# Kernel tuning notes

Measured on AMD Instinct MI355X. Metric: run time of the kernel, lower is better.

The kernel has to match this reference:

```python
import jax, jax.numpy as jnp
import numpy as np

B, L, E, H, D, DFF = 2, 2048, 1024, 16, 64, 4096
SCALE = D ** 0.5


def rmsnorm(x):
    # NOTE: original uses mean(x*x)**0.5 with no eps and no learned scale
    rms = jnp.sqrt(jnp.mean(x * x, axis=-1, keepdims=True))
    return x / rms


def alibi_matrix():
    i = jnp.arange(L)
    dists = -jnp.abs(i[None, :] - i[:, None]).astype(jnp.float32)  # [L, L]
    slopes = 2.0 ** (-jnp.linspace(1.0, 8.0, H))                   # [H]
    alibi = slopes[:, None, None] * dists                          # [H, L, L]
    causal = jnp.tril(jnp.ones((L, L), dtype=bool))
    return jnp.where(causal[None], alibi, -jnp.inf)[None]          # [1, H, L, L]


def setup_inputs() -> dict:
    key = jax.random.key(0)
    ks = jax.random.split(key, 16)
    s = 0.02
    return {
        "X": jax.random.normal(ks[0], (B, L, E), jnp.float32),
        "encoder_out": jax.random.normal(ks[1], (B, L, E), jnp.float32),
        # self-attention params
        "Wqkv": jax.random.normal(ks[2], (E, 3 * H * D), jnp.float32) * s,
        "bqkv": jnp.zeros((3 * H * D,), jnp.float32),
        "Wo_sa": jax.random.normal(ks[3], (H * D, E), jnp.float32) * s,
        "bo_sa": jnp.zeros((E,), jnp.float32),
        # cross-attention params (computed by torch module but its forward returns X, so unused)
        "Wq": jax.random.normal(ks[4], (E, H * D), jnp.float32) * s,
        "bq": jnp.zeros((H * D,), jnp.float32),
        "Wkv": jax.random.normal(ks[5], (E, 2 * H * D), jnp.float32) * s,
        "bkv": jnp.zeros((2 * H * D,), jnp.float32),
        "Wo_ca": jax.random.normal(ks[6], (H * D, E), jnp.float32) * s,
        "bo_ca": jnp.zeros((E,), jnp.float32),
        # GLU FFN params (bias=False)
        "Ww": jax.random.normal(ks[7], (E, DFF), jnp.float32) * s,
        "Wv": jax.random.normal(ks[8], (E, DFF), jnp.float32) * s,
        "Wout": jax.random.normal(ks[9], (DFF, E), jnp.float32) * s,
    }


def reference(X, encoder_out, Wqkv, bqkv, Wo_sa, bo_sa, Wq, bq, Wkv, bkv,
              Wo_ca, bo_ca, Ww, Wv, Wout):
    alibi = alibi_matrix()

    # ---- self-attention (pre-norm + residual) ----
    h = rmsnorm(X)
    qkv = (h @ Wqkv + bqkv).reshape(B, L, H, 3, D)
    Q, K, V = qkv[..., 0, :], qkv[..., 1, :], qkv[..., 2, :]      # [B, L, H, D]
    scores = jnp.einsum('blhd,bmhd->bhlm', Q, K) / SCALE + alibi  # [B, H, L, L]
    attn = jax.nn.softmax(scores, axis=-1)
    ctx = jnp.einsum('bhlm,bmhd->blhd', attn, V).reshape(B, L, H * D)
    X = X + ctx @ Wo_sa + bo_sa

    # ---- cross-attention stage ----
    # Faithful to source: CrossAttention.forward returns its input X (the
    # normalized tensor) rather than the attention output, so this block is
    # X + rmsnorm(X). Cross-attn params never affect the output.
    X = X + rmsnorm(X)

    # ---- GLU FFN (pre-norm + residual), exact (erf) GELU as in torch F.gelu ----
    h = rmsnorm(X)
    ff = jax.nn.gelu(h @ Ww, approximate=False) * (h @ Wv)
    X = X + ff @ Wout
    return X
```

## Files before the change

kernel.cpp:

```cpp
#include <hip/hip_runtime.h>

#define B_SZ 2
#define L_SEQ 2048
#define E_DIM 1024
#define NH 16
#define DH 64
#define DFF_DIM 4096
#define ROWS (B_SZ * L_SEQ)
#define NCID 80

typedef __attribute__((ext_vector_type(8))) short short8;
typedef __attribute__((ext_vector_type(4))) float f32x4;

__device__ __forceinline__ short f2bf(float f) {
  unsigned u = __builtin_bit_cast(unsigned, f);
  u = (u + 0x7FFFu + ((u >> 16) & 1u)) >> 16;
  return (short)u;
}
__device__ __forceinline__ float bf2f(short s) {
  unsigned u = ((unsigned)(unsigned short)s) << 16;
  return __builtin_bit_cast(float, u);
}

__device__ __forceinline__ void async_copy16(const void* g, void* l) {
  __builtin_amdgcn_global_load_lds(
      (const __attribute__((address_space(1))) void*)g,
      (__attribute__((address_space(3))) void*)l, 16, 0, 0);
}

__device__ __forceinline__ float block_sum256(float v) {
  __shared__ float sbuf[4];
#pragma unroll
  for (int off = 32; off > 0; off >>= 1) v += __shfl_xor(v, off, 64);
  int lane = threadIdx.x & 63, w = threadIdx.x >> 6;
  if (lane == 0) sbuf[w] = v;
  __syncthreads();
  return sbuf[0] + sbuf[1] + sbuf[2] + sbuf[3];
}

__global__ __launch_bounds__(256) void prep_all(
    const float* __restrict__ Wqkv, const float* __restrict__ Wo,
    const float* __restrict__ Ww, const float* __restrict__ Wv,
    const float* __restrict__ Wout, const float* __restrict__ X,
    short* __restrict__ WqkvT, short* __restrict__ WoT,
    short* __restrict__ Bcat, short* __restrict__ WoutT,
    short* __restrict__ H) {
  __shared__ float tile[32][33];
  int b = blockIdx.x;
  if (b < 16384) {
    const float* W;
    short* Wt;
    int K, N, poff, bx, by;
    if (b < 3072) {
      W = Wqkv; Wt = WqkvT; K = 1024; N = 3072; poff = -1;
      bx = b % 96; by = b / 96;
    } else if (b < 4096) {
      int c = b - 3072;
      W = Wo; Wt = WoT; K = 1024; N = 1024; poff = -1;
      bx = c & 31; by = c >> 5;
    } else if (b < 8192) {
      int c = b - 4096;
      W = Ww; Wt = Bcat; K = 1024; N = 4096; poff = 0;
      bx = c & 127; by = c >> 7;
    } else if (b < 12288) {
      int c = b - 8192;
      W = Wv; Wt = Bcat; K = 1024; N = 4096; poff = 64;
      bx = c & 127; by = c >> 7;
    } else {
      int c = b - 12288;
      W = Wout; Wt = WoutT; K = 4096; N = 1024; poff = -1;
      bx = c & 31; by = c >> 5;
    }
    int n0 = bx * 32, k0 = by * 32;
    int tx = threadIdx.x & 31, ty = threadIdx.x >> 5;
#pragma unroll
    for (int i = 0; i < 4; i++)
      tile[ty + 8 * i][tx] = W[(size_t)(k0 + ty + 8 * i) * N + n0 + tx];
    __syncthreads();
#pragma unroll
    for (int i = 0; i < 4; i++) {
      int n = n0 + ty + 8 * i;
      int orow = (poff < 0) ? n : ((n >> 6) * 128 + (n & 63) + poff);
      Wt[(size_t)orow * K + k0 + tx] = f2bf(tile[tx][ty + 8 * i]);
    }
  } else {
    size_t row = b - 16384;
    float4 v = ((const float4*)(X + row * E_DIM))[threadIdx.x];
    float ss = v.x * v.x + v.y * v.y + v.z * v.z + v.w * v.w;
    ss = block_sum256(ss);
    float inv = rsqrtf(ss * (1.0f / E_DIM));
    short* h = H + row * E_DIM + (size_t)threadIdx.x * 4;
    h[0] = f2bf(v.x * inv);
    h[1] = f2bf(v.y * inv);
    h[2] = f2bf(v.z * inv);
    h[3] = f2bf(v.w * inv);
  }
}

__global__ __launch_bounds__(256) void resid_rms_fused(
    const float* __restrict__ X, const float* __restrict__ P0,
    const float* __restrict__ P1, const float* __restrict__ bias,
    float* __restrict__ Xout, short* __restrict__ H) {
  size_t row = blockIdx.x;
  int t = threadIdx.x;
  float4 v = ((const float4*)(X + row * E_DIM))[t];
  float4 a = ((const float4*)(P0 + row * E_DIM))[t];
  float4 b = ((const float4*)(P1 + row * E_DIM))[t];
  float4 c = ((const float4*)bias)[t];
  v.x += a.x + b.x + c.x;
  v.y += a.y + b.y + c.y;
  v.z += a.z + b.z + c.z;
  v.w += a.w + b.w + c.w;
  float ss = v.x * v.x + v.y * v.y + v.z * v.z + v.w * v.w;
  ss = block_sum256(ss);
  float inv = rsqrtf(ss * (1.0f / E_DIM));
  float4 o;
  o.x = v.x * (1.0f + inv);
  o.y = v.y * (1.0f + inv);
  o.z = v.z * (1.0f + inv);
  o.w = v.w * (1.0f + inv);
  ((float4*)(Xout + row * E_DIM))[t] = o;
  short* h = H + row * E_DIM + (size_t)t * 4;
  h[0] = f2bf(v.x * inv);
  h[1] = f2bf(v.y * inv);
  h[2] = f2bf(v.z * inv);
  h[3] = f2bf(v.w * inv);
}

__global__ __launch_bounds__(256) void add2_k(const float* __restrict__ X2,
                                              const float* __restrict__ P0,
                                              const float* __restrict__ P1,
                                              float* __restrict__ out) {
  size_t i = (size_t)blockIdx.x * 256 + threadIdx.x;
  float4 v = ((const float4*)X2)[i];
  float4 a = ((const float4*)P0)[i];
  float4 b = ((const float4*)P1)[i];
  v.x += a.x + b.x;
  v.y += a.y + b.y;
  v.z += a.z + b.z;
  v.w += a.w + b.w;
  ((float4*)out)[i] = v;
}

__global__ __launch_bounds__(256, 2) void gemm_bt(
    const short* __restrict__ A, const short* __restrict__ Bt,
    const float* __restrict__ bias, const float* __restrict__ res,
    void* __restrict__ out, int M, int N, int K, int epi, int ksplit) {
  __shared__ short smem[128 * 32 * 4];
  short* As0 = smem;
  short* Bs0 = smem + 4096;
  short* As1 = smem + 8192;
  short* Bs1 = smem + 12288;
  int t = threadIdx.x;
  int lane = t & 63;
  int quad = lane >> 4, l16 = lane & 15;
  int wave = t >> 6;
  int wr = wave >> 1, wc = wave & 1;
  int m0 = blockIdx.y * 128, n0 = blockIdx.x * 128;
  int klen = K / ksplit;
  int kstart = blockIdx.z * klen;

  f32x4 acc[4][4];
#pragma unroll
  for (int i = 0; i < 4; i++)
#pragma unroll
    for (int j = 0; j < 4; j++) acc[i][j] = (f32x4){0.f, 0.f, 0.f, 0.f};

  for (int k0 = kstart; k0 < kstart + klen; k0 += 64) {
    __syncthreads();
#pragma unroll
    for (int p = 0; p < 2; p++) {
      int s = p * 256 + t;
      int mm = s >> 2, kk = (s & 3) * 8;
      const short* ag = A + (size_t)(m0 + mm) * K + k0 + kk;
      const short* bg = Bt + (size_t)(n0 + mm) * K + k0 + kk;
      async_copy16(ag, As0 + (size_t)s * 8);
      async_copy16(bg, Bs0 + (size_t)s * 8);
      async_copy16(ag + 32, As1 + (size_t)s * 8);
      async_copy16(bg + 32, Bs1 + (size_t)s * 8);
    }
    __syncthreads();
#pragma unroll
    for (int half = 0; half < 2; half++) {
      const short* As = half ? As1 : As0;
      const short* Bs = half ? Bs1 : Bs0;
      short8 af[4], bfv[4];
#pragma unroll
      for (int i = 0; i < 4; i++) {
        af[i] = *(const short8*)&As[(wr * 64 + i * 16 + l16) * 32 + quad * 8];
        bfv[i] = *(const short8*)&Bs[(wc * 64 + i * 16 + l16) * 32 + quad * 8];
      }
#pragma unroll
      for (int mi = 0; mi < 4; mi++)
#pragma unroll
        for (int ni = 0; ni < 4; ni++)
          acc[mi][ni] = __builtin_amdgcn_mfma_f32_16x16x32_bf16(
              af[mi], bfv[ni], acc[mi][ni], 0, 0, 0);
    }
  }

  if (epi == 5) {
    __syncthreads();
    short* xbuf = smem;
    if (wc == 0) {
#pragma unroll
      for (int mi = 0; mi < 4; mi++)
#pragma unroll
        for (int ni = 0; ni < 4; ni++)
#pragma unroll
          for (int r = 0; r < 4; r++) {
            int rowl = wr * 64 + mi * 16 + quad * 4 + r;
            float v = acc[mi][ni][r];
            float g = 0.5f * v * (1.0f + erff(v * 0.70710678118654752f));
            xbuf[rowl * 68 + ni * 16 + l16] = f2bf(g);
          }
    }
    __syncthreads();
    if (wc == 1) {
      short* FF = (short*)out;
#pragma unroll
      for (int mi = 0; mi < 4; mi++)
#pragma unroll
        for (int ni = 0; ni < 4; ni++)
#pragma unroll
          for (int r = 0; r < 4; r++) {
            int rowl = wr * 64 + mi * 16 + quad * 4 + r;
            int coll = ni * 16 + l16;
            float w = bf2f(xbuf[rowl * 68 + coll]);
            FF[(size_t)(m0 + rowl) * DFF_DIM + blockIdx.x * 64 + coll] =
                f2bf(w * acc[mi][ni][r]);
          }
    }
    return;
  }

#pragma unroll
  for (int mi = 0; mi < 4; mi++) {
#pragma unroll
    for (int ni = 0; ni < 4; ni++) {
      int col = n0 + wc * 64 + ni * 16 + l16;
      float bv = bias ? bias[col] : 0.0f;
#pragma unroll
      for (int r = 0; r < 4; r++) {
        int row = m0 + wr * 64 + mi * 16 + quad * 4 + r;
        size_t idx = (size_t)row * N + col;
        float v = acc[mi][ni][r] + bv;
        if (epi == 0) {
          ((short*)out)[idx] = f2bf(v);
        } else if (epi == 3) {
          ((float*)out)[idx] = v + res[idx];
        } else {
          float* po = (float*)out + (size_t)blockIdx.z * ((size_t)M * N);
          po[idx] = v;
        }
      }
    }
  }
}

__global__ __launch_bounds__(256) void kv_prep(const short* __restrict__ qkv,
                                               short* __restrict__ Kh,
                                               short* __restrict__ VTh) {
  int lt = blockIdx.x, bh = blockIdx.y;
  int b = bh >> 4, h = bh & 15;
  __shared__ short vtile[64 * 72];
  int t = threadIdx.x;
  int r = t >> 3, c = (t & 7) * 8;
  const short* base =
      qkv + (size_t)(b * L_SEQ + lt * 64) * (3 * NH * DH) + h * (3 * DH);
#pragma unroll
  for (int p = 0; p < 2; p++) {
    int row = r + p * 32;
    short8 kv = *(const short8*)(base + (size_t)row * (3 * NH * DH) + DH + c);
    *(short8*)(Kh + ((size_t)bh * L_SEQ + lt * 64 + row) * DH + c) = kv;
    short8 vv =
        *(const short8*)(base + (size_t)row * (3 * NH * DH) + 2 * DH + c);
    *(short8*)&vtile[row * 72 + c] = vv;
  }
  __syncthreads();
#pragma unroll
  for (int p = 0; p < 2; p++) {
    int d = r + p * 32;
    short8 o;
#pragma unroll
    for (int u = 0; u < 8; u++) o[u] = vtile[(c + u) * 72 + d];
    *(short8*)(VTh + ((size_t)bh * DH + d) * L_SEQ + lt * 64 + c) = o;
  }
}

__global__ __launch_bounds__(256) void attn_k(const short* __restrict__ qkv,
                                              const short* __restrict__ Kh,
                                              const short* __restrict__ VTh,
                                              float* __restrict__ OP,
                                              float* __restrict__ RS) {
  int cid = blockIdx.x;
  int bh = blockIdx.y;
  int b = bh >> 4, h = bh & 15;
  int qt, ch;
  if (cid < 8) {
    qt = cid; ch = 0;
  } else if (cid < 24) {
    qt = 8 + ((cid - 8) >> 1); ch = (cid - 8) & 1;
  } else if (cid < 48) {
    qt = 16 + (cid - 24) / 3; ch = (cid - 24) % 3;
  } else {
    qt = 24 + ((cid - 48) >> 2); ch = (cid - 48) & 3;
  }
  int t0 = ch * 8;
  int tend = min(t0 + 8, qt + 1);

  int t = threadIdx.x;
  int wave = t >> 6, lane = t & 63;
  int quad = lane >> 4, l16 = lane & 15;

  __shared__ short kt[64 * 72];
  __shared__ short vt[64 * 72];
  __shared__ short pb[4 * 16 * 70];

  const float slope = exp2f(-(1.0f + (7.0f / 15.0f) * (float)h));
  const size_t rowstride = 3 * NH * DH;
  const short* qbase = qkv + (size_t)(b * L_SEQ) * rowstride + h * (3 * DH);
  int iw = qt * 64 + wave * 16;

  short8 qf[2];
  {
    const short* qp = qbase + (size_t)(iw + l16) * rowstride + quad * 8;
    qf[0] = *(const short8*)(qp);
    qf[1] = *(const short8*)(qp + 32);
  }

  f32x4 o[4];
#pragma unroll
  for (int i = 0; i < 4; i++) o[i] = (f32x4){0.f, 0.f, 0.f, 0.f};
  float rs[4] = {0.f, 0.f, 0.f, 0.f};
  float crow[4];
  int irow[4];
#pragma unroll
  for (int r = 0; r < 4; r++) {
    irow[r] = iw + quad * 4 + r;
    crow[r] = -slope * (float)irow[r] - 8.0f;
  }

  int sr = t >> 3, sc = (t & 7) * 8;
  const short* kg = Kh + (size_t)bh * L_SEQ * DH;
  const short* vg = VTh + (size_t)bh * DH * L_SEQ;
  short8 kreg[2], vreg[2];
  auto loadKV = [&](int j0) {
    kreg[0] = *(const short8*)(kg + (size_t)(j0 + sr) * DH + sc);
    kreg[1] = *(const short8*)(kg + (size_t)(j0 + sr + 32) * DH + sc);
    vreg[0] = *(const short8*)(vg + (size_t)sr * L_SEQ + j0 + sc);
    vreg[1] = *(const short8*)(vg + (size_t)(sr + 32) * L_SEQ + j0 + sc);
  };
  loadKV(t0 * 64);

  short* pw = &pb[wave * 16 * 70];
  for (int tix = t0; tix < tend; ++tix) {
    int j0 = tix * 64;
    __syncthreads();
    *(short8*)&kt[sr * 72 + sc] = kreg[0];
    *(short8*)&kt[(sr + 32) * 72 + sc] = kreg[1];
    *(short8*)&vt[sr * 72 + sc] = vreg[0];
    *(short8*)&vt[(sr + 32) * 72 + sc] = vreg[1];
    __syncthreads();
    if (tix + 1 < tend) loadKV(j0 + 64);

    f32x4 s[4];
#pragma unroll
    for (int nt = 0; nt < 4; nt++) {
      f32x4 a = (f32x4){0.f, 0.f, 0.f, 0.f};
#pragma unroll
      for (int ks = 0; ks < 2; ks++) {
        short8 bf =
            *(const short8*)&kt[(nt * 16 + l16) * 72 + ks * 32 + quad * 8];
        a = __builtin_amdgcn_mfma_f32_16x16x32_bf16(qf[ks], bf, a, 0, 0, 0);
      }
      s[nt] = a;
    }
    bool diag = (tix == qt);
#pragma unroll
    for (int nt = 0; nt < 4; nt++) {
      int j = j0 + nt * 16 + l16;
      float jb = slope * (float)j;
#pragma unroll
      for (int r = 0; r < 4; r++) {
        float v = __builtin_fmaf(s[nt][r], 0.125f, jb + crow[r]);
        if (diag && j > irow[r]) v = -1e30f;
        float p = __expf(v);
        rs[r] += p;
        pw[(quad * 4 + r) * 70 + nt * 16 + l16] = f2bf(p);
      }
    }
    short8 pf[2];
    pf[0] = *(const short8*)&pw[l16 * 70 + quad * 8];
    pf[1] = *(const short8*)&pw[l16 * 70 + 32 + quad * 8];
#pragma unroll
    for (int nt = 0; nt < 4; nt++) {
#pragma unroll
      for (int ks = 0; ks < 2; ks++) {
        short8 bv =
            *(const short8*)&vt[(nt * 16 + l16) * 72 + ks * 32 + quad * 8];
        o[nt] = __builtin_amdgcn_mfma_f32_16x16x32_bf16(pf[ks], bv, o[nt], 0,
                                                        0, 0);
      }
    }
  }
  float* op = OP + ((size_t)bh * NCID + cid) * 64 * 64;
  float* rsp = RS + ((size_t)bh * NCID + cid) * 64;
#pragma unroll
  for (int r = 0; r < 4; r++) {
#pragma unroll
    for (int off = 1; off < 16; off <<= 1) rs[r] += __shfl_xor(rs[r], off, 64);
    int rowl = wave * 16 + quad * 4 + r;
#pragma unroll
    for (int nt = 0; nt < 4; nt++) op[rowl * 64 + nt * 16 + l16] = o[nt][r];
    if (l16 == 0) rsp[rowl] = rs[r];
  }
}

__global__ __launch_bounds__(256) void attn_merge(const float* __restrict__ OP,
                                                  const float* __restrict__ RS,
                                                  short* __restrict__ ctx) {
  int row = blockIdx.x;
  int b = row >> 11, i = row & 2047;
  int qt = i >> 6, rowin = i & 63;
  int base, nch;
  if (qt < 8) {
    base = qt; nch = 1;
  } else if (qt < 16) {
    base = 8 + 2 * (qt - 8); nch = 2;
  } else if (qt < 24) {
    base = 24 + 3 * (qt - 16); nch = 3;
  } else {
    base = 48 + 4 * (qt - 24); nch = 4;
  }
  int t = threadIdx.x;
  int col = t * 4;
  int h = col >> 6;
  int bh = b * NH + h;
  float4 o = {0.f, 0.f, 0.f, 0.f};
  float l = 0.f;
  for (int s = 0; s < nch; s++) {
    size_t cb = ((size_t)bh * NCID + base + s) * 64 + rowin;
    float4 v = *(const float4*)&OP[cb * 64 + (col & 63)];
    o.x += v.x;
    o.y += v.y;
    o.z += v.z;
    o.w += v.w;
    l += RS[cb];
  }
  float inv = 1.0f / l;
  short* dst = ctx + (size_t)row * (NH * DH) + col;
  dst[0] = f2bf(o.x * inv);
  dst[1] = f2bf(o.y * inv);
  dst[2] = f2bf(o.z * inv);
  dst[3] = f2bf(o.w * inv);
}

extern "C" void kernel_launch(void* const* d_in, const int* in_sizes, int n_in,
                              void* d_out, int out_size, void* d_ws,
                              size_t ws_size, hipStream_t stream) {
  const float* X = (const float*)d_in[0];
  const float* Wqkv = (const float*)d_in[2];
  const float* bqkv = (const float*)d_in[3];
  const float* Wo_sa = (const float*)d_in[4];
  const float* bo_sa = (const float*)d_in[5];
  const float* Ww = (const float*)d_in[12];
  const float* Wv = (const float*)d_in[13];
  const float* Wout = (const float*)d_in[14];

  char* ws = (char*)d_ws;
  auto take = [&](size_t bytes) {
    char* p = ws;
    ws += (bytes + 255) & ~(size_t)255;
    return p;
  };
  short* WqkvT = (short*)take((size_t)3 * NH * DH * E_DIM * 2);
  short* WoT = (short*)take((size_t)E_DIM * E_DIM * 2);
  short* Bcat = (short*)take((size_t)2 * DFF_DIM * E_DIM * 2);
  short* WoutT = (short*)take((size_t)E_DIM * DFF_DIM * 2);
  short* Hbuf = (short*)take((size_t)ROWS * E_DIM * 2);
  short* QKV = (short*)take((size_t)ROWS * 3 * NH * DH * 2);
  short* CTX = (short*)take((size_t)ROWS * NH * DH * 2);
  short* KVb = (short*)take((size_t)2 * B_SZ * NH * L_SEQ * DH * 2);
  float* X1 = (float*)take((size_t)ROWS * E_DIM * 4);
  short* FF = (short*)take((size_t)ROWS * DFF_DIM * 2);
  short* Kh = KVb;
  short* VTh = KVb + (size_t)B_SZ * NH * L_SEQ * DH;
  float* OP = (float*)X1;
  float* RS = OP + (size_t)B_SZ * NH * NCID * 64 * 64;
  float* Pwo = (float*)FF;
  float* Pwout = (float*)QKV;
  (void)ws_size;
  (void)in_sizes;
  (void)n_in;
  (void)out_size;

  dim3 blk(256);
  prep_all<<<16384 + ROWS, blk, 0, stream>>>(Wqkv, Wo_sa, Ww, Wv, Wout, X,
                                             WqkvT, WoT, Bcat, WoutT, Hbuf);
  gemm_bt<<<dim3(3072 / 128, ROWS / 128), blk, 0, stream>>>(
      Hbuf, WqkvT, bqkv, nullptr, QKV, ROWS, 3072, 1024, 0, 1);
  kv_prep<<<dim3(L_SEQ / 64, B_SZ * NH), blk, 0, stream>>>(QKV, Kh, VTh);
  attn_k<<<dim3(NCID, B_SZ * NH), blk, 0, stream>>>(QKV, Kh, VTh, OP, RS);
  attn_merge<<<ROWS, blk, 0, stream>>>(OP, RS, CTX);
  gemm_bt<<<dim3(1024 / 128, ROWS / 128, 2), blk, 0, stream>>>(
      CTX, WoT, nullptr, nullptr, Pwo, ROWS, 1024, 1024, 4, 2);
  resid_rms_fused<<<ROWS, blk, 0, stream>>>(
      X, Pwo, Pwo + (size_t)ROWS * E_DIM, bo_sa, X1, Hbuf);
  gemm_bt<<<dim3(2 * DFF_DIM / 128, ROWS / 128), blk, 0, stream>>>(
      Hbuf, Bcat, nullptr, nullptr, FF, ROWS, 2 * DFF_DIM, 1024, 5, 1);
  gemm_bt<<<dim3(1024 / 128, ROWS / 128, 2), blk, 0, stream>>>(
      FF, WoutT, nullptr, nullptr, Pwout, ROWS, 1024, 4096, 4, 2);
  add2_k<<<ROWS * E_DIM / (256 * 4), blk, 0, stream>>>(
      X1, Pwout, Pwout + (size_t)ROWS * E_DIM, (float*)d_out);
}
```

Measured before the change: 441.8 us.

## Write QKV directly in head-major layouts and fuse final residual via atomics

Splits the QKV weight into a Q/K part and a V part. The Q/K GEMM epilogue scatters into head-major Q and K buffers, and a second swapped-operand GEMM writes V already transposed, so the kv_prep kernel and the QKV round trip are removed. The final Wout split-K GEMM now atomically adds into the output, which already holds the residual written by resid_rms_fused, so add2_k is removed. The cost is scattered epilogue stores, an extra GEMM launch, and float atomics with nondeterministic summation order.

```diff
diff --git a/kernel.cpp b/kernel.cpp
--- a/kernel.cpp
+++ b/kernel.cpp
@@ -42,33 +42,33 @@
     const float* __restrict__ Wqkv, const float* __restrict__ Wo,
     const float* __restrict__ Ww, const float* __restrict__ Wv,
     const float* __restrict__ Wout, const float* __restrict__ X,
-    short* __restrict__ WqkvT, short* __restrict__ WoT,
-    short* __restrict__ Bcat, short* __restrict__ WoutT,
-    short* __restrict__ H) {
+    short* __restrict__ WqkT, short* __restrict__ Wv3T,
+    short* __restrict__ WoT, short* __restrict__ Bcat,
+    short* __restrict__ WoutT, short* __restrict__ H) {
   __shared__ float tile[32][33];
   int b = blockIdx.x;
   if (b < 16384) {
     const float* W;
+    int K, N, mode, bx, by;
     short* Wt;
-    int K, N, poff, bx, by;
     if (b < 3072) {
-      W = Wqkv; Wt = WqkvT; K = 1024; N = 3072; poff = -1;
+      W = Wqkv; Wt = nullptr; K = 1024; N = 3072; mode = 0;
       bx = b % 96; by = b / 96;
     } else if (b < 4096) {
       int c = b - 3072;
-      W = Wo; Wt = WoT; K = 1024; N = 1024; poff = -1;
+      W = Wo; Wt = WoT; K = 1024; N = 1024; mode = 1;
       bx = c & 31; by = c >> 5;
     } else if (b < 8192) {
       int c = b - 4096;
-      W = Ww; Wt = Bcat; K = 1024; N = 4096; poff = 0;
+      W = Ww; Wt = Bcat; K = 1024; N = 4096; mode = 2;
       bx = c & 127; by = c >> 7;
     } else if (b < 12288) {
       int c = b - 8192;
-      W = Wv; Wt = Bcat; K = 1024; N = 4096; poff = 64;
+      W = Wv; Wt = Bcat; K = 1024; N = 4096; mode = 3;
       bx = c & 127; by = c >> 7;
     } else {
       int c = b - 12288;
-      W = Wout; Wt = WoutT; K = 4096; N = 1024; poff = -1;
+      W = Wout; Wt = WoutT; K = 4096; N = 1024; mode = 1;
       bx = c & 31; by = c >> 5;
     }
     int n0 = bx * 32, k0 = by * 32;
@@ -80,8 +80,18 @@
 #pragma unroll
     for (int i = 0; i < 4; i++) {
       int n = n0 + ty + 8 * i;
-      int orow = (poff < 0) ? n : ((n >> 6) * 128 + (n & 63) + poff);
-      Wt[(size_t)orow * K + k0 + tx] = f2bf(tile[tx][ty + 8 * i]);
+      short val = f2bf(tile[tx][ty + 8 * i]);
+      if (mode == 0) {
+        int h = n / 192, rem = n - h * 192;
+        if (rem < 128)
+          WqkT[(size_t)(h * 128 + rem) * 1024 + k0 + tx] = val;
+        else
+          Wv3T[(size_t)(h * 64 + rem - 128) * 1024 + k0 + tx] = val;
+      } else {
+        int orow = (mode == 1) ? n
+                               : ((n >> 6) * 128 + (n & 63) + (mode == 3 ? 64 : 0));
+        Wt[(size_t)orow * K + k0 + tx] = val;
+      }
     }
   } else {
     size_t row = b - 16384;
@@ -127,25 +137,10 @@
   h[3] = f2bf(v.w * inv);
 }
 
-__global__ __launch_bounds__(256) void add2_k(const float* __restrict__ X2,
-                                              const float* __restrict__ P0,
-                                              const float* __restrict__ P1,
-                                              float* __restrict__ out) {
-  size_t i = (size_t)blockIdx.x * 256 + threadIdx.x;
-  float4 v = ((const float4*)X2)[i];
-  float4 a = ((const float4*)P0)[i];
-  float4 b = ((const float4*)P1)[i];
-  v.x += a.x + b.x;
-  v.y += a.y + b.y;
-  v.z += a.z + b.z;
-  v.w += a.w + b.w;
-  ((float4*)out)[i] = v;
-}
-
 __global__ __launch_bounds__(256, 2) void gemm_bt(
     const short* __restrict__ A, const short* __restrict__ Bt,
-    const float* __restrict__ bias, const float* __restrict__ res,
-    void* __restrict__ out, int M, int N, int K, int epi, int ksplit) {
+    const float* __restrict__ bias, void* __restrict__ out,
+    void* __restrict__ out2, int M, int N, int K, int epi, int ksplit) {
   __shared__ short smem[128 * 32 * 4];
   short* As0 = smem;
   short* Bs0 = smem + 4096;
@@ -239,56 +234,34 @@
 #pragma unroll
     for (int ni = 0; ni < 4; ni++) {
       int col = n0 + wc * 64 + ni * 16 + l16;
-      float bv = bias ? bias[col] : 0.0f;
 #pragma unroll
       for (int r = 0; r < 4; r++) {
         int row = m0 + wr * 64 + mi * 16 + quad * 4 + r;
-        size_t idx = (size_t)row * N + col;
-        float v = acc[mi][ni][r] + bv;
-        if (epi == 0) {
-          ((short*)out)[idx] = f2bf(v);
-        } else if (epi == 3) {
-          ((float*)out)[idx] = v + res[idx];
+        float v = acc[mi][ni][r];
+        if (epi == 4) {
+          float* po = (float*)out + (size_t)blockIdx.z * ((size_t)M * N);
+          po[(size_t)row * N + col] = v;
+        } else if (epi == 6) {
+          v += bias[(col >> 7) * 192 + (col & 127)];
+          int h = col >> 7, d = col & 63;
+          short* dst = ((col >> 6) & 1) ? (short*)out2 : (short*)out;
+          int bb = row >> 11, l = row & 2047;
+          dst[((size_t)(bb * NH + h) * L_SEQ + l) * DH + d] = f2bf(v);
+        } else if (epi == 7) {
+          v += bias[(row >> 6) * 192 + 128 + (row & 63)];
+          int bb = col >> 11, l = col & 2047;
+          ((short*)out)[((size_t)(bb * NH + (row >> 6)) * DH + (row & 63)) *
+                            L_SEQ +
+                        l] = f2bf(v);
         } else {
-          float* po = (float*)out + (size_t)blockIdx.z * ((size_t)M * N);
-          po[idx] = v;
+          unsafeAtomicAdd((float*)out + (size_t)row * N + col, v);
         }
       }
     }
   }
 }
 
-__global__ __launch_bounds__(256) void kv_prep(const short* __restrict__ qkv,
-                                               short* __restrict__ Kh,
-                                               short* __restrict__ VTh) {
-  int lt = blockIdx.x, bh = blockIdx.y;
-  int b = bh >> 4, h = bh & 15;
-  __shared__ short vtile[64 * 72];
-  int t = threadIdx.x;
-  int r = t >> 3, c = (t & 7) * 8;
-  const short* base =
-      qkv + (size_t)(b * L_SEQ + lt * 64) * (3 * NH * DH) + h * (3 * DH);
-#pragma unroll
-  for (int p = 0; p < 2; p++) {
-    int row = r + p * 32;
-    short8 kv = *(const short8*)(base + (size_t)row * (3 * NH * DH) + DH + c);
-    *(short8*)(Kh + ((size_t)bh * L_SEQ + lt * 64 + row) * DH + c) = kv;
-    short8 vv =
-        *(const short8*)(base + (size_t)row * (3 * NH * DH) + 2 * DH + c);
-    *(short8*)&vtile[row * 72 + c] = vv;
-  }
-  __syncthreads();
-#pragma unroll
-  for (int p = 0; p < 2; p++) {
-    int d = r + p * 32;
-    short8 o;
-#pragma unroll
-    for (int u = 0; u < 8; u++) o[u] = vtile[(c + u) * 72 + d];
-    *(short8*)(VTh + ((size_t)bh * DH + d) * L_SEQ + lt * 64 + c) = o;
-  }
-}
-
-__global__ __launch_bounds__(256) void attn_k(const short* __restrict__ qkv,
+__global__ __launch_bounds__(256) void attn_k(const short* __restrict__ Qh,
                                               const short* __restrict__ Kh,
                                               const short* __restrict__ VTh,
                                               float* __restrict__ OP,
@@ -318,13 +291,11 @@
   __shared__ short pb[4 * 16 * 70];
 
   const float slope = exp2f(-(1.0f + (7.0f / 15.0f) * (float)h));
-  const size_t rowstride = 3 * NH * DH;
-  const short* qbase = qkv + (size_t)(b * L_SEQ) * rowstride + h * (3 * DH);
   int iw = qt * 64 + wave * 16;
 
   short8 qf[2];
   {
-    const short* qp = qbase + (size_t)(iw + l16) * rowstride + quad * 8;
+    const short* qp = Qh + ((size_t)bh * L_SEQ + iw + l16) * DH + quad * 8;
     qf[0] = *(const short8*)(qp);
     qf[1] = *(const short8*)(qp + 32);
   }
@@ -474,22 +445,22 @@
     ws += (bytes + 255) & ~(size_t)255;
     return p;
   };
-  short* WqkvT = (short*)take((size_t)3 * NH * DH * E_DIM * 2);
+  short* WqkT = (short*)take((size_t)2048 * 1024 * 2);
+  short* Wv3T = (short*)take((size_t)1024 * 1024 * 2);
   short* WoT = (short*)take((size_t)E_DIM * E_DIM * 2);
   short* Bcat = (short*)take((size_t)2 * DFF_DIM * E_DIM * 2);
   short* WoutT = (short*)take((size_t)E_DIM * DFF_DIM * 2);
   short* Hbuf = (short*)take((size_t)ROWS * E_DIM * 2);
-  short* QKV = (short*)take((size_t)ROWS * 3 * NH * DH * 2);
+  short* Qh = (short*)take((size_t)ROWS * NH * DH * 2);
   short* CTX = (short*)take((size_t)ROWS * NH * DH * 2);
   short* KVb = (short*)take((size_t)2 * B_SZ * NH * L_SEQ * DH * 2);
-  float* X1 = (float*)take((size_t)ROWS * E_DIM * 4);
-  short* FF = (short*)take((size_t)ROWS * DFF_DIM * 2);
+  char* big = take((size_t)48 * 1024 * 1024);
   short* Kh = KVb;
   short* VTh = KVb + (size_t)B_SZ * NH * L_SEQ * DH;
-  float* OP = (float*)X1;
+  float* OP = (float*)big;
   float* RS = OP + (size_t)B_SZ * NH * NCID * 64 * 64;
+  short* FF = (short*)(big + (size_t)16 * 1024 * 1024);
   float* Pwo = (float*)FF;
-  float* Pwout = (float*)QKV;
   (void)ws_size;
   (void)in_sizes;
   (void)n_in;
@@ -497,20 +468,20 @@
 
   dim3 blk(256);
   prep_all<<<16384 + ROWS, blk, 0, stream>>>(Wqkv, Wo_sa, Ww, Wv, Wout, X,
-                                             WqkvT, WoT, Bcat, WoutT, Hbuf);
-  gemm_bt<<<dim3(3072 / 128, ROWS / 128), blk, 0, stream>>>(
-      Hbuf, WqkvT, bqkv, nullptr, QKV, ROWS, 3072, 1024, 0, 1);
-  kv_prep<<<dim3(L_SEQ / 64, B_SZ * NH), blk, 0, stream>>>(QKV, Kh, VTh);
-  attn_k<<<dim3(NCID, B_SZ * NH), blk, 0, stream>>>(QKV, Kh, VTh, OP, RS);
+                                             WqkT, Wv3T, WoT, Bcat, WoutT,
+                                             Hbuf);
+  gemm_bt<<<dim3(2048 / 128, ROWS / 128), blk, 0, stream>>>(
+      Hbuf, WqkT, bqkv, Qh, Kh, ROWS, 2048, 1024, 6, 1);
+  gemm_bt<<<dim3(ROWS / 128, 1024 / 128), blk, 0, stream>>>(
+      Wv3T, Hbuf, bqkv, VTh, nullptr, 1024, ROWS, 1024, 7, 1);
+  attn_k<<<dim3(NCID, B_SZ * NH), blk, 0, stream>>>(Qh, Kh, VTh, OP, RS);
   attn_merge<<<ROWS, blk, 0, stream>>>(OP, RS, CTX);
   gemm_bt<<<dim3(1024 / 128, ROWS / 128, 2), blk, 0, stream>>>(
-      CTX, WoT, nullptr, nullptr, Pwo, ROWS, 1024, 1024, 4, 2);
+      CTX, WoT, nullptr, Pwo, nullptr, ROWS, 1024, 1024, 4, 2);
   resid_rms_fused<<<ROWS, blk, 0, stream>>>(
-      X, Pwo, Pwo + (size_t)ROWS * E_DIM, bo_sa, X1, Hbuf);
+      X, Pwo, Pwo + (size_t)ROWS * E_DIM, bo_sa, (float*)d_out, Hbuf);
   gemm_bt<<<dim3(2 * DFF_DIM / 128, ROWS / 128), blk, 0, stream>>>(
-      Hbuf, Bcat, nullptr, nullptr, FF, ROWS, 2 * DFF_DIM, 1024, 5, 1);
+      Hbuf, Bcat, nullptr, FF, nullptr, ROWS, 2 * DFF_DIM, 1024, 5, 1);
   gemm_bt<<<dim3(1024 / 128, ROWS / 128, 2), blk, 0, stream>>>(
-      FF, WoutT, nullptr, nullptr, Pwout, ROWS, 1024, 4096, 4, 2);
-  add2_k<<<ROWS * E_DIM / (256 * 4), blk, 0, stream>>>(
-      X1, Pwout, Pwout + (size_t)ROWS * E_DIM, (float*)d_out);
-}
+      FF, WoutT, nullptr, d_out, nullptr, ROWS, 1024, 4096, 8, 2);
+}
```

New measurement: 455.0 us. 3.0% more time.
